# Kernel optimization log

Hardware: AMD Instinct MI355X
Metric: run time of the kernel (lower is better)

The kernel has to match this reference:

```python
import jax, jax.numpy as jnp
import numpy as np

GRID = 1024  # grid resolution -> V = GRID*GRID vertices


def _grid_mesh(G):
    """Build a triangulated GxG grid mesh; return laplacian directed edges and
    normal-consistency interior-edge index quadruples [v0, v1, v2, v3] where
    (v0,v1) is the shared edge and v2, v3 the opposite vertices of the two faces."""
    V = G * G
    i, j = np.meshgrid(np.arange(G - 1), np.arange(G - 1), indexing="ij")
    a = (i * G + j).ravel(); b = (i * G + j + 1).ravel()
    c = ((i + 1) * G + j).ravel(); d = ((i + 1) * G + j + 1).ravel()
    faces = np.concatenate([np.stack([a, b, c], 1), np.stack([b, d, c], 1)], 0).astype(np.int64)
    # half-edges with opposite vertex per face
    e = np.concatenate([faces[:, [0, 1]], faces[:, [1, 2]], faces[:, [2, 0]]], 0)
    opp = np.concatenate([faces[:, 2], faces[:, 0], faces[:, 1]], 0)
    e = np.sort(e, 1)
    key = e[:, 0] * V + e[:, 1]
    order = np.argsort(key, kind="stable")
    ks, opps = key[order], opp[order]
    dup = np.nonzero(ks[1:] == ks[:-1])[0]  # edges shared by exactly two faces
    nc_idx = np.stack([ks[dup] // V, ks[dup] % V, opps[dup], opps[dup + 1]], 1)
    uk = np.unique(key)
    src, dst = uk // V, uk % V
    lap_src = np.concatenate([src, dst])
    lap_dst = np.concatenate([dst, src])
    return lap_src.astype(np.int32), lap_dst.astype(np.int32), nc_idx.astype(np.int32)


def setup_inputs() -> dict:
    key = jax.random.key(0)
    k1, k2 = jax.random.split(key)
    G = GRID; V = G * G
    lap_src, lap_dst, nc_idx = _grid_mesh(G)
    verts = jax.random.normal(k1, (V, 3), jnp.float32)          # template_mesh.verts_packed()
    deform_verts = jax.random.normal(k2, (V, 3), jnp.float32) * 0.05  # nn.Parameter
    return {
        "verts": verts,
        "deform_verts": deform_verts,
        "lap_src": jnp.asarray(lap_src),
        "lap_dst": jnp.asarray(lap_dst),
        "nc_idx": jnp.asarray(nc_idx),
        "batch_size": 4,
    }


def reference(verts, deform_verts, lap_src, lap_dst, nc_idx, batch_size):
    V = verts.shape[0]
    new_verts = verts + deform_verts  # Meshes.offset_verts

    # mesh_laplacian_smoothing(method='uniform'):
    # per-vertex (mean of neighbors - vertex), loss = mean ||.||
    nbr_sum = jax.ops.segment_sum(new_verts[lap_src], lap_dst, num_segments=V)
    deg = jax.ops.segment_sum(jnp.ones(lap_src.shape, jnp.float32), lap_dst, num_segments=V)
    lap = nbr_sum / jnp.maximum(deg, 1.0)[:, None] - new_verts
    laplacian_loss = jnp.linalg.norm(lap, axis=1).mean()

    # mesh_normal_consistency: for each interior edge (v0,v1) with opposite
    # verts v2, v3: n0 = (v1-v0) x (v2-v0), n1 = -(v1-v0) x (v3-v0),
    # loss = mean(1 - cos(n0, n1))
    v0 = new_verts[nc_idx[:, 0]]; v1 = new_verts[nc_idx[:, 1]]
    v2 = new_verts[nc_idx[:, 2]]; v3 = new_verts[nc_idx[:, 3]]
    e01 = v1 - v0
    n0 = jnp.cross(e01, v2 - v0)
    n1 = -jnp.cross(e01, v3 - v0)
    cos = (n0 * n1).sum(-1) / jnp.maximum(
        jnp.linalg.norm(n0, axis=-1) * jnp.linalg.norm(n1, axis=-1), 1e-8)
    flatten_loss = (1.0 - cos).mean()

    # Meshes.extend(batch_size): replicate deformed mesh verts
    batched_verts = jnp.broadcast_to(new_verts, (batch_size, V, 3))
    return batched_verts, laplacian_loss, flatten_loss
```

## Files before the change

kernel.cpp:

```cpp
#include <hip/hip_runtime.h>

#define G 1024
#define V (G * G)
#define NBLK 4096
#define NEDGE 3137541.0f

struct F3 { float x, y, z; };

__device__ inline F3 ldnv(const float* __restrict__ v, const float* __restrict__ d, int id) {
    int b = 3 * id;
    F3 r;
    r.x = v[b]     + d[b];
    r.y = v[b + 1] + d[b + 1];
    r.z = v[b + 2] + d[b + 2];
    return r;
}

__device__ inline float omc(F3 v0, F3 v1, F3 v2, F3 v3) {
    float ex = v1.x - v0.x, ey = v1.y - v0.y, ez = v1.z - v0.z;
    float ax = v2.x - v0.x, ay = v2.y - v0.y, az = v2.z - v0.z;
    float bx = v3.x - v0.x, by = v3.y - v0.y, bz = v3.z - v0.z;
    float n0x = ey * az - ez * ay;
    float n0y = ez * ax - ex * az;
    float n0z = ex * ay - ey * ax;
    float n1x = ez * by - ey * bz;
    float n1y = ex * bz - ez * bx;
    float n1z = ey * bx - ex * by;
    float dd = n0x * n1x + n0y * n1y + n0z * n1z;
    float m0 = sqrtf(n0x * n0x + n0y * n0y + n0z * n0z);
    float m1 = sqrtf(n1x * n1x + n1y * n1y + n1z * n1z);
    float c  = dd / fmaxf(m0 * m1, 1e-8f);
    return 1.0f - c;
}

__global__ __launch_bounds__(256) void fused_kernel(const float* __restrict__ verts,
                                                    const float* __restrict__ dv,
                                                    float* __restrict__ out,
                                                    float* __restrict__ wsp) {
    int b = blockIdx.x;
    int L  = ((b & 7) << 9) | (b >> 3);
    int id = (L << 8) + (int)threadIdx.x;
    int i  = id >> 10;
    int j  = id & (G - 1);

    F3 self = ldnv(verts, dv, id);

    int o = 3 * id;
    out[o]             = self.x; out[o + 1]         = self.y; out[o + 2]         = self.z;
    out[o + 3 * V]     = self.x; out[o + 3 * V + 1] = self.y; out[o + 3 * V + 2] = self.z;
    out[o + 6 * V]     = self.x; out[o + 6 * V + 1] = self.y; out[o + 6 * V + 2] = self.z;
    out[o + 9 * V]     = self.x; out[o + 9 * V + 1] = self.y; out[o + 9 * V + 2] = self.z;

    bool hasL = (j > 0), hasR = (j < G - 1), hasU = (i > 0), hasD = (i < G - 1);

    F3 pL{0,0,0}, pR{0,0,0}, pU{0,0,0}, pD{0,0,0}, pUR{0,0,0}, pDL{0,0,0}, pDR{0,0,0};
    if (hasL)          pL  = ldnv(verts, dv, id - 1);
    if (hasR)          pR  = ldnv(verts, dv, id + 1);
    if (hasU)          pU  = ldnv(verts, dv, id - G);
    if (hasD)          pD  = ldnv(verts, dv, id + G);
    if (hasU && hasR)  pUR = ldnv(verts, dv, id - G + 1);
    if (hasD && hasL)  pDL = ldnv(verts, dv, id + G - 1);
    if (hasD && hasR)  pDR = ldnv(verts, dv, id + G + 1);

    int   degi = (int)hasL + (int)hasR + (int)hasU + (int)hasD
               + (int)(hasU && hasR) + (int)(hasD && hasL);
    float inv  = 1.0f / (float)degi;
    float sx = pL.x + pR.x + pU.x + pD.x + pUR.x + pDL.x;
    float sy = pL.y + pR.y + pU.y + pD.y + pUR.y + pDL.y;
    float sz = pL.z + pR.z + pU.z + pD.z + pUR.z + pDL.z;
    float lx = sx * inv - self.x;
    float ly = sy * inv - self.y;
    float lz = sz * inv - self.z;
    float lap_n = sqrtf(lx * lx + ly * ly + lz * lz);

    float fl = 0.0f;
    if (hasD && hasR) {
        fl = omc(pR, pD, self, pDR);
        if (hasU) fl += omc(self, pR, pD, pUR);
        if (hasL) fl += omc(self, pD, pR, pDL);
    }

    for (int off = 32; off > 0; off >>= 1) {
        lap_n += __shfl_down(lap_n, off);
        fl    += __shfl_down(fl, off);
    }
    __shared__ float red[8];
    int lane = threadIdx.x & 63, wv = threadIdx.x >> 6;
    if (lane == 0) { red[wv] = lap_n; red[4 + wv] = fl; }
    __syncthreads();
    if (threadIdx.x == 0) {
        wsp[blockIdx.x]        = red[0] + red[1] + red[2] + red[3];
        wsp[NBLK + blockIdx.x] = red[4] + red[5] + red[6] + red[7];
    }
}

__global__ __launch_bounds__(256) void finalize_kernel(const float* __restrict__ wsp,
                                                       float* __restrict__ out) {
    float s = 0.0f, f = 0.0f;
    for (int k = threadIdx.x; k < NBLK; k += 256) {
        s += wsp[k];
        f += wsp[NBLK + k];
    }
    for (int off = 32; off > 0; off >>= 1) {
        s += __shfl_down(s, off);
        f += __shfl_down(f, off);
    }
    __shared__ float red[8];
    int lane = threadIdx.x & 63, wv = threadIdx.x >> 6;
    if (lane == 0) { red[wv] = s; red[4 + wv] = f; }
    __syncthreads();
    if (threadIdx.x == 0) {
        float ts = red[0] + red[1] + red[2] + red[3];
        float tf = red[4] + red[5] + red[6] + red[7];
        out[12 * V]     = ts / (float)V;
        out[12 * V + 1] = tf / NEDGE;
    }
}

extern "C" void kernel_launch(void* const* d_in, const int* in_sizes, int n_in,
                              void* d_out, int out_size, void* d_ws, size_t ws_size,
                              hipStream_t stream) {
    const float* verts = (const float*)d_in[0];
    const float* dv    = (const float*)d_in[1];
    float* out = (float*)d_out;
    float* wsp = (float*)d_ws;

    fused_kernel<<<NBLK, 256, 0, stream>>>(verts, dv, out, wsp);
    finalize_kernel<<<1, 256, 0, stream>>>(wsp, out);
}
```

Baseline: 174.3 us.

## Stage three vertex rows in LDS per block with vectorized loads and nontemporal stores

Each block now handles one full grid row. It loads the row above, the row itself and the row below into shared memory using float4 loads, adding verts and deform_verts once per element. The replicated output is written with vectorized nontemporal stores, and the stencil neighbours are read from LDS instead of being re-gathered from global memory. This removes the redundant strided global loads and the scalar stride-3 accesses. In exchange each row is loaded three times across blocks, there are fewer blocks (1024), and there is a barrier before compute.

New measurement: 154.2 us. 1.13x faster.

```diff
diff --git a/kernel.cpp b/kernel.cpp
--- a/kernel.cpp
+++ b/kernel.cpp
@@ -1,18 +1,20 @@
 #include <hip/hip_runtime.h>
 
 #define G 1024
+#define ROWF 3072
+#define ROWF4 768
 #define V (G * G)
-#define NBLK 4096
+#define NBLK 1024
+#define COPY4 786432
 #define NEDGE 3137541.0f
+
+typedef float v4 __attribute__((ext_vector_type(4)));
 
 struct F3 { float x, y, z; };
 
-__device__ inline F3 ldnv(const float* __restrict__ v, const float* __restrict__ d, int id) {
-    int b = 3 * id;
-    F3 r;
-    r.x = v[b]     + d[b];
-    r.y = v[b + 1] + d[b + 1];
-    r.z = v[b + 2] + d[b + 2];
+__device__ inline F3 ldl(const float* __restrict__ nv, int slot, int col) {
+    int b = slot * ROWF + 3 * col;
+    F3 r; r.x = nv[b]; r.y = nv[b + 1]; r.z = nv[b + 2];
     return r;
 }
 
@@ -38,59 +40,85 @@
                                                     float* __restrict__ out,
                                                     float* __restrict__ wsp) {
     int b = blockIdx.x;
-    int L  = ((b & 7) << 9) | (b >> 3);
-    int id = (L << 8) + (int)threadIdx.x;
-    int i  = id >> 10;
-    int j  = id & (G - 1);
+    int i = ((b & 7) << 7) | (b >> 3);
+    int t = threadIdx.x;
 
-    F3 self = ldnv(verts, dv, id);
+    __shared__ v4 nv4[3 * ROWF4];
+    const float* nv = (const float*)nv4;
 
-    int o = 3 * id;
-    out[o]             = self.x; out[o + 1]         = self.y; out[o + 2]         = self.z;
-    out[o + 3 * V]     = self.x; out[o + 3 * V + 1] = self.y; out[o + 3 * V + 2] = self.z;
-    out[o + 6 * V]     = self.x; out[o + 6 * V + 1] = self.y; out[o + 6 * V + 2] = self.z;
-    out[o + 9 * V]     = self.x; out[o + 9 * V + 1] = self.y; out[o + 9 * V + 2] = self.z;
+    const v4* vin4 = (const v4*)verts;
+    const v4* dvi4 = (const v4*)dv;
 
-    bool hasL = (j > 0), hasR = (j < G - 1), hasU = (i > 0), hasD = (i < G - 1);
+    #pragma unroll
+    for (int s = 0; s < 3; ++s) {
+        int r = i + s - 1;
+        r = r < 0 ? 0 : (r > G - 1 ? G - 1 : r);
+        int base = r * ROWF4;
+        #pragma unroll
+        for (int k = 0; k < 3; ++k) {
+            int idx = t + (k << 8);
+            nv4[s * ROWF4 + idx] = vin4[base + idx] + dvi4[base + idx];
+        }
+    }
+    __syncthreads();
 
-    F3 pL{0,0,0}, pR{0,0,0}, pU{0,0,0}, pD{0,0,0}, pUR{0,0,0}, pDL{0,0,0}, pDR{0,0,0};
-    if (hasL)          pL  = ldnv(verts, dv, id - 1);
-    if (hasR)          pR  = ldnv(verts, dv, id + 1);
-    if (hasU)          pU  = ldnv(verts, dv, id - G);
-    if (hasD)          pD  = ldnv(verts, dv, id + G);
-    if (hasU && hasR)  pUR = ldnv(verts, dv, id - G + 1);
-    if (hasD && hasL)  pDL = ldnv(verts, dv, id + G - 1);
-    if (hasD && hasR)  pDR = ldnv(verts, dv, id + G + 1);
+    bool hasU = (i > 0), hasD = (i < G - 1);
 
-    int   degi = (int)hasL + (int)hasR + (int)hasU + (int)hasD
-               + (int)(hasU && hasR) + (int)(hasD && hasL);
-    float inv  = 1.0f / (float)degi;
-    float sx = pL.x + pR.x + pU.x + pD.x + pUR.x + pDL.x;
-    float sy = pL.y + pR.y + pU.y + pD.y + pUR.y + pDL.y;
-    float sz = pL.z + pR.z + pU.z + pD.z + pUR.z + pDL.z;
-    float lx = sx * inv - self.x;
-    float ly = sy * inv - self.y;
-    float lz = sz * inv - self.z;
-    float lap_n = sqrtf(lx * lx + ly * ly + lz * lz);
+    v4* out4 = (v4*)out;
+    #pragma unroll
+    for (int k = 0; k < 3; ++k) {
+        int idx = t + (k << 8);
+        v4 val  = nv4[ROWF4 + idx];
+        int oi  = i * ROWF4 + idx;
+        __builtin_nontemporal_store(val, &out4[oi]);
+        __builtin_nontemporal_store(val, &out4[oi + COPY4]);
+        __builtin_nontemporal_store(val, &out4[oi + 2 * COPY4]);
+        __builtin_nontemporal_store(val, &out4[oi + 3 * COPY4]);
+    }
 
-    float fl = 0.0f;
-    if (hasD && hasR) {
-        fl = omc(pR, pD, self, pDR);
-        if (hasU) fl += omc(self, pR, pD, pUR);
-        if (hasL) fl += omc(self, pD, pR, pDL);
+    float lap_sum = 0.0f, fl_sum = 0.0f;
+
+    #pragma unroll
+    for (int k = 0; k < 4; ++k) {
+        int j = t + (k << 8);
+        bool hasL = (j > 0), hasR = (j < G - 1);
+
+        F3 self = ldl(nv, 1, j);
+        F3 pL{0,0,0}, pR{0,0,0}, pU{0,0,0}, pD{0,0,0}, pUR{0,0,0}, pDL{0,0,0}, pDR{0,0,0};
+        if (hasL)          pL  = ldl(nv, 1, j - 1);
+        if (hasR)          pR  = ldl(nv, 1, j + 1);
+        if (hasU)          pU  = ldl(nv, 0, j);
+        if (hasD)          pD  = ldl(nv, 2, j);
+        if (hasU && hasR)  pUR = ldl(nv, 0, j + 1);
+        if (hasD && hasL)  pDL = ldl(nv, 2, j - 1);
+        if (hasD && hasR)  pDR = ldl(nv, 2, j + 1);
+
+        int   degi = (int)hasL + (int)hasR + (int)hasU + (int)hasD
+                   + (int)(hasU && hasR) + (int)(hasD && hasL);
+        float inv  = 1.0f / (float)degi;
+        float lx = (pL.x + pR.x + pU.x + pD.x + pUR.x + pDL.x) * inv - self.x;
+        float ly = (pL.y + pR.y + pU.y + pD.y + pUR.y + pDL.y) * inv - self.y;
+        float lz = (pL.z + pR.z + pU.z + pD.z + pUR.z + pDL.z) * inv - self.z;
+        lap_sum += sqrtf(lx * lx + ly * ly + lz * lz);
+
+        if (hasD && hasR) {
+            fl_sum += omc(pR, pD, self, pDR);
+            if (hasU) fl_sum += omc(self, pR, pD, pUR);
+            if (hasL) fl_sum += omc(self, pD, pR, pDL);
+        }
     }
 
     for (int off = 32; off > 0; off >>= 1) {
-        lap_n += __shfl_down(lap_n, off);
-        fl    += __shfl_down(fl, off);
+        lap_sum += __shfl_down(lap_sum, off);
+        fl_sum  += __shfl_down(fl_sum, off);
     }
     __shared__ float red[8];
-    int lane = threadIdx.x & 63, wv = threadIdx.x >> 6;
-    if (lane == 0) { red[wv] = lap_n; red[4 + wv] = fl; }
+    int lane = t & 63, wv = t >> 6;
+    if (lane == 0) { red[wv] = lap_sum; red[4 + wv] = fl_sum; }
     __syncthreads();
-    if (threadIdx.x == 0) {
-        wsp[blockIdx.x]        = red[0] + red[1] + red[2] + red[3];
-        wsp[NBLK + blockIdx.x] = red[4] + red[5] + red[6] + red[7];
+    if (t == 0) {
+        wsp[b]        = red[0] + red[1] + red[2] + red[3];
+        wsp[NBLK + b] = red[4] + red[5] + red[6] + red[7];
     }
 }
 
@@ -110,10 +138,8 @@
     if (lane == 0) { red[wv] = s; red[4 + wv] = f; }
     __syncthreads();
     if (threadIdx.x == 0) {
-        float ts = red[0] + red[1] + red[2] + red[3];
-        float tf = red[4] + red[5] + red[6] + red[7];
-        out[12 * V]     = ts / (float)V;
-        out[12 * V + 1] = tf / NEDGE;
+        out[12 * V]     = (red[0] + red[1] + red[2] + red[3]) / (float)V;
+        out[12 * V + 1] = (red[4] + red[5] + red[6] + red[7]) / NEDGE;
     }
 }
 
```
